# Kernel tuning notes

Measured on AMD Instinct MI355X. Metric: run time of the kernel, lower is better.

## Reference

```python
import jax, jax.numpy as jnp
import numpy as np

NINP, NC, NH = 34, 128, 512
B, S, T = 64, 2048, 400
EPS = 1e-10


def _lstm_cell(x, h, c, Wih, Whh, bih, bhh):
    # torch.nn.LSTMCell gate order: i, f, g, o
    g = x @ Wih.T + bih + h @ Whh.T + bhh
    i, f, gg, o = jnp.split(g, 4, axis=1)
    c2 = jax.nn.sigmoid(f) * c + jax.nn.sigmoid(i) * jnp.tanh(gg)
    h2 = jax.nn.sigmoid(o) * jnp.tanh(c2)
    return h2, c2


def _attend(keys, values, mask, query):
    # energy: [B, S]; mask: [B, S] float 0/1
    energy = jnp.einsum('bc,bsc->bs', query, keys) * mask
    energy = energy - (1.0 - mask) * 1e6
    e = jnp.exp(energy - energy.max(axis=1, keepdims=True)) * mask
    att = e / e.sum(axis=1, keepdims=True)
    ctx = jnp.einsum('bs,bsc->bc', att, values)
    return att, ctx


def setup_inputs() -> dict:
    key = jax.random.key(0)
    ks = jax.random.split(key, 32)
    def rn(k, shape, scale=0.05):
        return (jax.random.normal(k, shape) * scale).astype(jnp.float32)
    inp = {
        'keys': rn(ks[0], (B, S, NC), 1.0),
        'values': rn(ks[1], (B, S, NC), 1.0),
        'lens': jax.random.randint(ks[2], (B,), S // 2, S + 1),
        'inputs': jax.random.randint(ks[3], (B, T), 0, NINP),
        'emb': rn(ks[4], (NINP, NC)),
        'wq': rn(ks[5], (NC, NH)), 'bq': jnp.zeros((NC,), jnp.float32),
        'wc': rn(ks[6], (NC, NH + NC)), 'bc': jnp.zeros((NC,), jnp.float32),
        'b_out': jnp.zeros((NINP,), jnp.float32),
    }
    in_sizes = [2 * NC, NH, NH]
    for l in range(3):
        inp['w%d_ih' % l] = rn(ks[7 + 4 * l], (4 * NH, in_sizes[l]))
        inp['w%d_hh' % l] = rn(ks[8 + 4 * l], (4 * NH, NH))
        inp['b%d_ih' % l] = jnp.zeros((4 * NH,), jnp.float32)
        inp['b%d_hh' % l] = jnp.zeros((4 * NH,), jnp.float32)
        inp['h0_%d' % l] = jnp.zeros((NH,), jnp.float32)  # ALSTMCell h0 param (zero init)
        inp['c0_%d' % l] = jnp.zeros((NH,), jnp.float32)
    return inp


def reference(keys, values, lens, inputs, emb, wq, bq, wc, bc, b_out,
              w0_ih, w0_hh, b0_ih, b0_hh, h0_0, c0_0,
              w1_ih, w1_hh, b1_ih, b1_hh, h0_1, c0_1,
              w2_ih, w2_hh, b2_ih, b2_hh, h0_2, c0_2):
    mask = (jnp.arange(S)[None, :] < lens[:, None]).astype(keys.dtype)  # [B,S]
    h1 = jnp.broadcast_to(h0_0[None], (B, NH)); c1 = jnp.broadcast_to(c0_0[None], (B, NH))
    h2 = jnp.broadcast_to(h0_1[None], (B, NH)); c2 = jnp.broadcast_to(c0_1[None], (B, NH))
    h3 = jnp.broadcast_to(h0_2[None], (B, NH)); c3 = jnp.broadcast_to(c0_2[None], (B, NH))
    # initial attention from last layer's h0 (matches torch forward)
    query0 = h3 @ wq.T + bq
    _, ctx = _attend(keys, values, mask, query0)
    # precompute gumbel noise for all T steps: -log(eps - log(U + eps))
    U = jax.random.uniform(jax.random.key(1), (T, B, NINP), dtype=jnp.float32)
    gnoise = -jnp.log(EPS - jnp.log(U + EPS))

    def step(carry, xs):
        h1, c1, h2, c2, h3, c3, ctx = carry
        tok, gn = xs
        x = jnp.concatenate([emb[tok], ctx], axis=1)  # [B, 2*NC]
        h1, c1 = _lstm_cell(x, h1, c1, w0_ih, w0_hh, b0_ih, b0_hh)
        h2, c2 = _lstm_cell(h1, h2, c2, w1_ih, w1_hh, b1_ih, b1_hh)
        h3, c3 = _lstm_cell(h2, h3, c3, w2_ih, w2_hh, b2_ih, b2_hh)
        q = h3 @ wq.T + bq
        att, ctx = _attend(keys, values, mask, q)
        z = jax.nn.leaky_relu(jnp.concatenate([h3, ctx], axis=1) @ wc.T + bc, 0.01)
        logit = z @ emb.T + b_out  # tied output weight = embedding
        gen = jnp.argmax(logit + gn, axis=1)
        return (h1, c1, h2, c2, h3, c3, ctx), (logit, att, gen)

    _, (logits, attentions, generated) = jax.lax.scan(
        step, (h1, c1, h2, c2, h3, c3, ctx), (inputs.T, gnoise))
    return logits, attentions, generated
```

## Files before the change

kernel.cpp:

```cpp
#include <hip/hip_runtime.h>

#define NINP 34
#define NCC  128
#define NHH  512
#define BBB  64
#define SSS  2048
#define TTT  400
#define GEPS 1e-10f

#define GDIM 512
#define NTHR 256
#define NCHK 8
#define SCHK 256

#define JAX_PARTITIONABLE 1

#define OFF_H   0
#define OFF_C   196608
#define OFF_CTX 294912
#define OFF_ML  303104
#define OFF_P   303616

#define SY_ROOT 0
#define SY_GEN  16
#define SY_LEAFC(l) (256 + 8 * (l))
#define SY_LEAFG(l) (512 + 8 * (l))
#define SY_BF(b)    (1024 + 8 * (b))
#define SY_MF(b)    (1536 + 8 * (b))

struct Params {
  const float* keys; const float* values;
  const int* lens;  const int* toks;
  const float* emb; const float* wq; const float* bq;
  const float* wc;  const float* bc; const float* bout;
  const float* wih[3]; const float* whh[3];
  const float* bih[3]; const float* bhh[3];
  const float* h0[3];  const float* c0[3];
  float* out_logits; float* out_att; float* out_gen;
  float* wsf; unsigned* sync;
};

__device__ __forceinline__ float4 ld4(const float* p) { return *(const float4*)p; }
__device__ __forceinline__ float sigf(float x) { return 1.0f / (1.0f + expf(-x)); }

__device__ __forceinline__ unsigned aload(const unsigned* p) {
  return __hip_atomic_load(p, __ATOMIC_RELAXED, __HIP_MEMORY_SCOPE_AGENT);
}
__device__ __forceinline__ unsigned aadd(unsigned* p, unsigned v) {
  return __hip_atomic_fetch_add(p, v, __ATOMIC_RELAXED, __HIP_MEMORY_SCOPE_AGENT);
}
__device__ __forceinline__ void astore(unsigned* p, unsigned v) {
  __hip_atomic_store(p, v, __ATOMIC_RELAXED, __HIP_MEMORY_SCOPE_AGENT);
}
__device__ __forceinline__ float ldc(const float* p) {
  unsigned u = __hip_atomic_load((const unsigned*)p, __ATOMIC_RELAXED, __HIP_MEMORY_SCOPE_AGENT);
  return __uint_as_float(u);
}
__device__ __forceinline__ void stc(float* p, float v) {
  __hip_atomic_store((unsigned*)p, __float_as_uint(v), __ATOMIC_RELAXED, __HIP_MEMORY_SCOPE_AGENT);
}
__device__ __forceinline__ float4 ld4c(const float* p) {
  unsigned long long a = __hip_atomic_load((const unsigned long long*)p,
                                           __ATOMIC_RELAXED, __HIP_MEMORY_SCOPE_AGENT);
  unsigned long long b = __hip_atomic_load(((const unsigned long long*)p) + 1,
                                           __ATOMIC_RELAXED, __HIP_MEMORY_SCOPE_AGENT);
  float4 r;
  r.x = __uint_as_float((unsigned)a); r.y = __uint_as_float((unsigned)(a >> 32));
  r.z = __uint_as_float((unsigned)b); r.w = __uint_as_float((unsigned)(b >> 32));
  return r;
}
__device__ __forceinline__ void wait_vm0() {
  asm volatile("s_waitcnt vmcnt(0)" ::: "memory");
}
__device__ __forceinline__ void cbar() { asm volatile("" ::: "memory"); }

__device__ void gbar(unsigned* sync, unsigned& epoch, int bid) {
  wait_vm0();
  __syncthreads();
  if (threadIdx.x == 0) {
    epoch++;
    const int leaf = bid >> 4;
    const bool leader = (bid & 15) == 0;
    if (aadd(&sync[SY_LEAFC(leaf)], 1u) == 16u * epoch - 1u) {
      if (aadd(&sync[SY_ROOT], 1u) == 32u * epoch - 1u)
        astore(&sync[SY_GEN], epoch);
    }
    if (leader) {
      while (aload(&sync[SY_GEN]) < epoch) __builtin_amdgcn_s_sleep(1);
      astore(&sync[SY_LEAFG(leaf)], epoch);
    } else {
      while (aload(&sync[SY_LEAFG(leaf)]) < epoch) __builtin_amdgcn_s_sleep(1);
    }
  }
  __syncthreads();
  cbar();
}

__device__ __forceinline__ void waitflag(unsigned* p, unsigned target) {
  if (threadIdx.x == 0) {
    while (aload(p) < target) __builtin_amdgcn_s_sleep(2);
  }
  __syncthreads();
  cbar();
}
__device__ __forceinline__ void postflag(unsigned* p) {
  wait_vm0();
  __syncthreads();
  if (threadIdx.x == 0) aadd(p, 1u);
}

__device__ __forceinline__ void tfr(unsigned& x0, unsigned& x1, int r) {
  x0 += x1; x1 = (x1 << r) | (x1 >> (32 - r)); x1 ^= x0;
}
__device__ unsigned threefry_bits(unsigned idx) {
  const unsigned k0 = 0u, k1 = 1u;
  const unsigned k2 = 0x1BD11BDAu ^ k0 ^ k1;
#if JAX_PARTITIONABLE
  unsigned x0 = 0u, x1 = idx;
#else
  const unsigned half = (TTT * BBB * NINP) / 2;
  const bool lo = idx < half;
  unsigned x0 = lo ? idx : idx - half;
  unsigned x1 = lo ? idx + half : idx;
#endif
  x0 += k0; x1 += k1;
  tfr(x0,x1,13); tfr(x0,x1,15); tfr(x0,x1,26); tfr(x0,x1,6);
  x0 += k1; x1 += k2 + 1u;
  tfr(x0,x1,17); tfr(x0,x1,29); tfr(x0,x1,16); tfr(x0,x1,24);
  x0 += k2; x1 += k0 + 2u;
  tfr(x0,x1,13); tfr(x0,x1,15); tfr(x0,x1,26); tfr(x0,x1,6);
  x0 += k0; x1 += k1 + 3u;
  tfr(x0,x1,17); tfr(x0,x1,29); tfr(x0,x1,16); tfr(x0,x1,24);
  x0 += k1; x1 += k2 + 4u;
  tfr(x0,x1,13); tfr(x0,x1,15); tfr(x0,x1,26); tfr(x0,x1,6);
  x0 += k2; x1 += k0 + 5u;
#if JAX_PARTITIONABLE
  return x0 ^ x1;
#else
  return lo ? x0 : x1;
#endif
}
__device__ __forceinline__ float gumbel(unsigned idx) {
  unsigned bits = threefry_bits(idx);
  float u = __uint_as_float((bits >> 9) | 0x3f800000u) - 1.0f;
  u = fmaxf(u, 0.0f);
  return -logf(GEPS - logf(u + GEPS));
}

template<int L>
__device__ void lstm_layer(const Params& p, int t, const float* hin, float* hout,
                           float* sh, int up, int bh, int tid) {
  const float* hin_l = hin + L * BBB * NHH + (size_t)bh * 32 * NHH;
  float* houtl = hout + L * BBB * NHH;
  float* cl = p.wsf + OFF_C + L * BBB * NHH;
  const float* xlow = (L == 0) ? (const float*)0
                               : (hout + (L - 1) * BBB * NHH + (size_t)bh * 32 * NHH);

  const int insz = (L == 0) ? (2 * NCC) : NHH;
  const int nx = insz >> 7;
  const int nch = nx + 4;

  const int rhat = tid >> 5;
  const int bloc = tid & 31;
  const int g = rhat >> 1, jh = rhat & 1;
  const int j = 2 * up + jh;
  const int row = g * NHH + j;
  const float* wr  = p.wih[L] + (size_t)row * insz;
  const float* wr2 = p.whh[L] + (size_t)row * NHH;

  float* xb0 = sh;
  float* xb1 = sh + 4224;
  const int kk  = (tid & 31) << 2;
  const int rb0 = tid >> 5;

  float4 pf[4];
  auto issue = [&](int cc) {
#pragma unroll
    for (int it = 0; it < 4; ++it) {
      const int rb = rb0 + (it << 3);
      const int gb = bh * 32 + rb;
      const bool isx = cc < nx;
      const int off = (isx ? cc : cc - nx) << 7;
      if (L == 0) {
        if (isx) pf[it] = (cc == 0)
            ? ld4(p.emb + (size_t)p.toks[gb * TTT + t] * NCC + kk)
            : ld4c(p.wsf + OFF_CTX + gb * NCC + kk);
        else pf[it] = ld4c(hin_l + (size_t)rb * NHH + off + kk);
      } else {
        pf[it] = isx ? ld4c(xlow + (size_t)rb * NHH + off + kk)
                     : ld4c(hin_l + (size_t)rb * NHH + off + kk);
      }
    }
  };
  auto commit = [&](float* buf) {
#pragma unroll
    for (int it = 0; it < 4; ++it)
      *(float4*)&buf[(rb0 + (it << 3)) * 132 + kk] = pf[it];
  };

  float acc = p.bih[L][row] + p.bhh[L][row];
  float s0 = 0.f, s1 = 0.f, s2 = 0.f, s3 = 0.f;

  issue(0);
  commit(xb0);
  __syncthreads();
  for (int cc = 0; cc < nch; ++cc) {
    if (cc + 1 < nch) issue(cc + 1);
    const bool isx = cc < nx;
    const int off = (isx ? cc : cc - nx) << 7;
    const float* wp = (isx ? wr : wr2) + off;
    const float* xr = ((cc & 1) ? xb1 : xb0) + bloc * 132;
#pragma unroll 8
    for (int k = 0; k < 128; k += 4) {
      float4 w = ld4(wp + k);
      float4 x = ld4(xr + k);
      s0 = fmaf(w.x, x.x, s0); s1 = fmaf(w.y, x.y, s1);
      s2 = fmaf(w.z, x.z, s2); s3 = fmaf(w.w, x.w, s3);
    }
    if (cc + 1 < nch) commit((cc & 1) ? xb0 : xb1);
    __syncthreads();
  }
  acc += (s0 + s1) + (s2 + s3);

  float* gl = sh + 8448;
  gl[rhat * 32 + bloc] = acc;
  __syncthreads();
  if (tid < 64) {
    const int jh2 = tid >> 5, b2 = tid & 31;
    const int b = bh * 32 + b2;
    const int jj = 2 * up + jh2;
    const float iv = gl[(0 + jh2) * 32 + b2];
    const float fv = gl[(2 + jh2) * 32 + b2];
    const float gv = gl[(4 + jh2) * 32 + b2];
    const float ov = gl[(6 + jh2) * 32 + b2];
    const float cold = cl[(size_t)b * NHH + jj];
    const float cnew = sigf(fv) * cold + sigf(iv) * tanhf(gv);
    const float hnew = sigf(ov) * tanhf(cnew);
    cl[(size_t)b * NHH + jj] = cnew;
    stc(&houtl[(size_t)b * NHH + jj], hnew);
  }
}

__device__ void attend_phase(const Params& p, int a, int t, const float* h3,
                             float* sh, int bid, int tid, bool wout) {
  float* wsf = p.wsf;
  unsigned* sync = p.sync;
  const int b  = (bid & 7) * 8 + (bid >> 6);
  const int ch = (bid >> 3) & 7;
  const int sbase = ch * SCHK;

  float* us  = sh + 8704;
  float* qs  = sh + 9344;
  float* ps  = sh + 9472;
  float* red = sh + 9728;
  float* zs  = sh + 10784;
  float* lg  = sh + 10912;

  if (tid < 128) *(float4*)&us[tid * 4] = ld4c(h3 + (size_t)b * NHH + tid * 4);
  __syncthreads();
  if (tid < NCC) {
    const float* wr = p.wq + (size_t)tid * NHH;
    float s0 = 0.f, s1 = 0.f, s2 = 0.f, s3 = 0.f;
#pragma unroll 8
    for (int k = 0; k < NHH; k += 4) {
      float4 w = ld4(wr + k);
      s0 = fmaf(w.x, us[k],     s0); s1 = fmaf(w.y, us[k + 1], s1);
      s2 = fmaf(w.z, us[k + 2], s2); s3 = fmaf(w.w, us[k + 3], s3);
    }
    qs[tid] = p.bq[tid] + (s0 + s1) + (s2 + s3);
  }
  const int lenb = p.lens[b];
  __syncthreads();

  const int s = sbase + tid;
  const float* kr = p.keys + ((size_t)b * SSS + s) * NCC;
  float e0 = 0.f, e1 = 0.f, e2 = 0.f, e3 = 0.f;
#pragma unroll 8
  for (int c = 0; c < NCC; c += 4) {
    float4 kv = ld4(kr + c);
    e0 = fmaf(qs[c],     kv.x, e0); e1 = fmaf(qs[c + 1], kv.y, e1);
    e2 = fmaf(qs[c + 2], kv.z, e2); e3 = fmaf(qs[c + 3], kv.w, e3);
  }
  float e = (e0 + e1) + (e2 + e3);
  const bool msk = s < lenb;
  e = msk ? e : -1e6f;

  float mx = e;
#pragma unroll
  for (int off = 32; off; off >>= 1) mx = fmaxf(mx, __shfl_xor(mx, off));
  if ((tid & 63) == 0) red[tid >> 6] = mx;
  __syncthreads();
  const float mc = fmaxf(fmaxf(red[0], red[1]), fmaxf(red[2], red[3]));
  const float pv = msk ? expf(e - mc) : 0.f;
  ps[tid] = pv;
  float ls = pv;
#pragma unroll
  for (int off = 32; off; off >>= 1) ls += __shfl_xor(ls, off);
  if ((tid & 63) == 0) red[4 + (tid >> 6)] = ls;
  __syncthreads();
  const float lc = (red[4] + red[5]) + (red[6] + red[7]);

  const int c4 = (tid & 31) << 2;
  const int sg = tid >> 5;
  float r0 = 0.f, r1 = 0.f, r2 = 0.f, r3 = 0.f;
  const float* vb = p.values + ((size_t)b * SSS + sbase + sg * 32) * NCC + c4;
#pragma unroll 4
  for (int i2 = 0; i2 < 32; ++i2) {
    const float pw = ps[sg * 32 + i2];
    float4 vv = ld4(vb + (size_t)i2 * NCC);
    r0 = fmaf(pw, vv.x, r0); r1 = fmaf(pw, vv.y, r1);
    r2 = fmaf(pw, vv.z, r2); r3 = fmaf(pw, vv.w, r3);
  }
  __syncthreads();
  *(float4*)&red[sg * 132 + c4] = make_float4(r0, r1, r2, r3);
  __syncthreads();
  float* pout = wsf + OFF_P + ((size_t)b * NCHK + ch) * 132;
  if (tid < NCC) {
    float sum = 0.f;
#pragma unroll
    for (int sg2 = 0; sg2 < 8; ++sg2) sum += red[sg2 * 132 + tid];
    stc(&pout[4 + tid], sum);
  }
  if (tid == 0) { stc(&pout[0], mc); stc(&pout[1], lc); }
  postflag(&sync[SY_BF(b)]);

  float gm = 0.f, gL = 1.f;
  if (ch == 0) {
    waitflag(&sync[SY_BF(b)], (unsigned)(NCHK * (a + 1)));
    const float* pb = wsf + OFF_P + (size_t)b * NCHK * 132;
    if (tid < 8)       red[tid] = ldc(&pb[tid * 132]);
    else if (tid < 16) red[tid] = ldc(&pb[(tid - 8) * 132 + 1]);
    __syncthreads();
    float m = red[0];
#pragma unroll
    for (int i = 1; i < 8; ++i) m = fmaxf(m, red[i]);
    float L = 0.f;
#pragma unroll
    for (int i = 0; i < 8; ++i) L += red[8 + i] * expf(red[i] - m);
    gm = m; gL = L;
    if (tid < NCC) {
      float v = 0.f;
#pragma unroll
      for (int c2 = 0; c2 < NCHK; ++c2)
        v += ldc(&pb[c2 * 132 + 4 + tid]) * expf(red[c2] - m);
      v /= L;
      stc(&wsf[OFF_CTX + b * NCC + tid], v);
      us[NHH + tid] = v;
    }
    if (tid == 0) { stc(&wsf[OFF_ML + b * 8], m); stc(&wsf[OFF_ML + b * 8 + 1], L); }
    postflag(&sync[SY_MF(b)]);
  } else if (wout) {
    waitflag(&sync[SY_MF(b)], (unsigned)(a + 1));
    gm = ldc(&wsf[OFF_ML + b * 8]);
    gL = ldc(&wsf[OFF_ML + b * 8 + 1]);
  }

  if (wout) {
    float* ao = p.out_att + ((size_t)t * BBB + b) * SSS;
    ao[s] = (msk ? expf(e - gm) : 0.f) / gL;
    if (ch == 0) {
      if (tid < NCC) {
        const float* wr = p.wc + (size_t)tid * (NHH + NCC);
        float s0 = 0.f, s1 = 0.f, s2 = 0.f, s3 = 0.f;
#pragma unroll 8
        for (int k = 0; k < NHH + NCC; k += 4) {
          float4 w = ld4(wr + k);
          s0 = fmaf(w.x, us[k],     s0); s1 = fmaf(w.y, us[k + 1], s1);
          s2 = fmaf(w.z, us[k + 2], s2); s3 = fmaf(w.w, us[k + 3], s3);
        }
        float z = (s0 + s1) + (s2 + s3) + p.bc[tid];
        zs[tid] = (z >= 0.f) ? z : 0.01f * z;
      }
      __syncthreads();
      if (tid < NINP) {
        const float* er = p.emb + tid * NCC;
        float s0 = 0.f, s1 = 0.f, s2 = 0.f, s3 = 0.f;
#pragma unroll 8
        for (int k = 0; k < NCC; k += 4) {
          float4 w = ld4(er + k);
          s0 = fmaf(w.x, zs[k],     s0); s1 = fmaf(w.y, zs[k + 1], s1);
          s2 = fmaf(w.z, zs[k + 2], s2); s3 = fmaf(w.w, zs[k + 3], s3);
        }
        const float lgt = (s0 + s1) + (s2 + s3) + p.bout[tid];
        p.out_logits[((size_t)t * BBB + b) * NINP + tid] = lgt;
        lg[tid] = lgt + gumbel((unsigned)(t * (BBB * NINP) + b * NINP + tid));
      }
      __syncthreads();
      if (tid == 0) {
        float bv = lg[0]; int bix = 0;
        for (int i = 1; i < NINP; ++i) if (lg[i] > bv) { bv = lg[i]; bix = i; }
        p.out_gen[t * BBB + b] = (float)bix;
      }
    }
  }
}

extern "C" __global__ void __launch_bounds__(NTHR, 2)
decoder_kernel(Params p) {
  __shared__ float sh[11008];
  const int bid = blockIdx.x;
  const int tid = threadIdx.x;
  const int up = (bid & 7) * 32 + (bid >> 4);
  const int bh = (bid >> 3) & 1;
  unsigned epoch = 0;
  unsigned* sync = p.sync;
  float* wsf = p.wsf;

  if (tid < 192) {
    const int l = tid >> 6, u = tid & 63;
    const int jh = u >> 5, b2 = u & 31;
    const int b = bh * 32 + b2;
    const int j = 2 * up + jh;
    stc(&wsf[OFF_H + ((size_t)l * BBB + b) * NHH + j], p.h0[l][j]);
    wsf[OFF_C + ((size_t)l * BBB + b) * NHH + j] = p.c0[l][j];
  }
  gbar(sync, epoch, bid);

  attend_phase(p, 0, -1, wsf + OFF_H + 2 * BBB * NHH, sh, bid, tid, false);
  gbar(sync, epoch, bid);

  for (int t = 0; t < TTT; ++t) {
    const float* hin = wsf + OFF_H + ((t & 1) ? 3 * BBB * NHH : 0);
    float* hout      = wsf + OFF_H + ((t & 1) ? 0 : 3 * BBB * NHH);

    lstm_layer<0>(p, t, hin, hout, sh, up, bh, tid);
    gbar(sync, epoch, bid);
    lstm_layer<1>(p, t, hin, hout, sh, up, bh, tid);
    gbar(sync, epoch, bid);
    lstm_layer<2>(p, t, hin, hout, sh, up, bh, tid);
    gbar(sync, epoch, bid);
    attend_phase(p, t + 1, t, hout + 2 * BBB * NHH, sh, bid, tid, true);
    gbar(sync, epoch, bid);
  }
}

extern "C" void kernel_launch(void* const* d_in, const int* in_sizes, int n_in,
                              void* d_out, int out_size, void* d_ws, size_t ws_size,
                              hipStream_t stream) {
  Params p;
  p.keys   = (const float*)d_in[0];
  p.values = (const float*)d_in[1];
  p.lens   = (const int*)d_in[2];
  p.toks   = (const int*)d_in[3];
  p.emb    = (const float*)d_in[4];
  p.wq     = (const float*)d_in[5];
  p.bq     = (const float*)d_in[6];
  p.wc     = (const float*)d_in[7];
  p.bc     = (const float*)d_in[8];
  p.bout   = (const float*)d_in[9];
  for (int l = 0; l < 3; ++l) {
    p.wih[l] = (const float*)d_in[10 + 6 * l];
    p.whh[l] = (const float*)d_in[11 + 6 * l];
    p.bih[l] = (const float*)d_in[12 + 6 * l];
    p.bhh[l] = (const float*)d_in[13 + 6 * l];
    p.h0[l]  = (const float*)d_in[14 + 6 * l];
    p.c0[l]  = (const float*)d_in[15 + 6 * l];
  }
  float* out = (float*)d_out;
  p.out_logits = out;
  p.out_att    = out + (size_t)TTT * BBB * NINP;
  p.out_gen    = out + (size_t)TTT * BBB * NINP + (size_t)TTT * BBB * SSS;
  p.sync = (unsigned*)d_ws;
  p.wsf  = (float*)((char*)d_ws + 8192);

  hipMemsetAsync(d_ws, 0, 8192, stream);
  decoder_kernel<<<dim3(GDIM), dim3(NTHR), 0, stream>>>(p);
}
```

Measured before the change: 49.78 ms.

## Replace post-attention grid barrier with per-half context flags and triple-buffer LSTM staging

Removes the grid-wide barrier after each attention phase. Layer-0 LSTM blocks now wait on a per-batch-half counter that the attention merge blocks bump when they publish ctx, so layer 0 can start its hidden-state chunks before all attention work finishes. The LSTM input staging moves from double to triple buffering with two register prefetch sets, which deepens the prefetch and raises shared memory use. This risks less occupancy and ordering hazards, since attention-output blocks may still be running when the LSTM reuses shared memory and workspace.

```diff
diff --git a/kernel.cpp b/kernel.cpp
--- a/kernel.cpp
+++ b/kernel.cpp
@@ -25,6 +25,7 @@
 #define SY_GEN  16
 #define SY_LEAFC(l) (256 + 8 * (l))
 #define SY_LEAFG(l) (512 + 8 * (l))
+#define SY_CTXH(h)  (768 + 64 * (h))
 #define SY_BF(b)    (1024 + 8 * (b))
 #define SY_MF(b)    (1536 + 8 * (b))
 
@@ -107,6 +108,11 @@
   wait_vm0();
   __syncthreads();
   if (threadIdx.x == 0) aadd(p, 1u);
+}
+__device__ __forceinline__ void postflag2(unsigned* p0, unsigned* p1) {
+  wait_vm0();
+  __syncthreads();
+  if (threadIdx.x == 0) { aadd(p0, 1u); aadd(p1, 1u); }
 }
 
 __device__ __forceinline__ void tfr(unsigned& x0, unsigned& x1, int r) {
@@ -149,16 +155,16 @@
 
 template<int L>
 __device__ void lstm_layer(const Params& p, int t, const float* hin, float* hout,
-                           float* sh, int up, int bh, int tid) {
+                           float* sh, int up, int bh, int tid, unsigned* sync) {
   const float* hin_l = hin + L * BBB * NHH + (size_t)bh * 32 * NHH;
   float* houtl = hout + L * BBB * NHH;
   float* cl = p.wsf + OFF_C + L * BBB * NHH;
   const float* xlow = (L == 0) ? (const float*)0
                                : (hout + (L - 1) * BBB * NHH + (size_t)bh * 32 * NHH);
 
-  const int insz = (L == 0) ? (2 * NCC) : NHH;
-  const int nx = insz >> 7;
-  const int nch = nx + 4;
+  constexpr int insz = (L == 0) ? (2 * NCC) : NHH;
+  constexpr int nx = insz >> 7;
+  constexpr int nch = nx + 4;
 
   const int rhat = tid >> 5;
   const int bloc = tid & 31;
@@ -168,13 +174,14 @@
   const float* wr  = p.wih[L] + (size_t)row * insz;
   const float* wr2 = p.whh[L] + (size_t)row * NHH;
 
-  float* xb0 = sh;
-  float* xb1 = sh + 4224;
+  float* const xb0 = sh;
+  float* const xb1 = sh + 4224;
+  float* const xb2 = sh + 8448;
   const int kk  = (tid & 31) << 2;
   const int rb0 = tid >> 5;
 
-  float4 pf[4];
-  auto issue = [&](int cc) {
+  float4 pfA[4], pfB[4];
+  auto issue = [&](float4 (&pf)[4], int cc) {
 #pragma unroll
     for (int it = 0; it < 4; ++it) {
       const int rb = rb0 + (it << 3);
@@ -192,7 +199,7 @@
       }
     }
   };
-  auto commit = [&](float* buf) {
+  auto commit = [&](float4 (&pf)[4], float* buf) {
 #pragma unroll
     for (int it = 0; it < 4; ++it)
       *(float4*)&buf[(rb0 + (it << 3)) * 132 + kk] = pf[it];
@@ -201,15 +208,21 @@
   float acc = p.bih[L][row] + p.bhh[L][row];
   float s0 = 0.f, s1 = 0.f, s2 = 0.f, s3 = 0.f;
 
-  issue(0);
-  commit(xb0);
-  __syncthreads();
+  issue(pfA, 0);
+  if (L == 0) {
+    waitflag(&sync[SY_CTXH(bh)], 32u * (unsigned)(t + 1));
+  }
+  commit(pfA, xb0);
+  issue(pfB, 1);
+  __syncthreads();
+#pragma unroll
   for (int cc = 0; cc < nch; ++cc) {
-    if (cc + 1 < nch) issue(cc + 1);
+    if (cc + 2 < nch) issue((cc & 1) ? pfB : pfA, cc + 2);
     const bool isx = cc < nx;
     const int off = (isx ? cc : cc - nx) << 7;
     const float* wp = (isx ? wr : wr2) + off;
-    const float* xr = ((cc & 1) ? xb1 : xb0) + bloc * 132;
+    float* const bufc = (cc % 3 == 0) ? xb0 : (cc % 3 == 1) ? xb1 : xb2;
+    const float* xr = bufc + bloc * 132;
 #pragma unroll 8
     for (int k = 0; k < 128; k += 4) {
       float4 w = ld4(wp + k);
@@ -217,12 +230,15 @@
       s0 = fmaf(w.x, x.x, s0); s1 = fmaf(w.y, x.y, s1);
       s2 = fmaf(w.z, x.z, s2); s3 = fmaf(w.w, x.w, s3);
     }
-    if (cc + 1 < nch) commit((cc & 1) ? xb0 : xb1);
+    if (cc + 1 < nch) {
+      float* const bufn = ((cc + 1) % 3 == 0) ? xb0 : ((cc + 1) % 3 == 1) ? xb1 : xb2;
+      commit(((cc + 1) & 1) ? pfB : pfA, bufn);
+    }
     __syncthreads();
   }
   acc += (s0 + s1) + (s2 + s3);
 
-  float* gl = sh + 8448;
+  float* gl = sh + 12672;
   gl[rhat * 32 + bloc] = acc;
   __syncthreads();
   if (tid < 64) {
@@ -249,12 +265,12 @@
   const int ch = (bid >> 3) & 7;
   const int sbase = ch * SCHK;
 
-  float* us  = sh + 8704;
-  float* qs  = sh + 9344;
-  float* ps  = sh + 9472;
-  float* red = sh + 9728;
-  float* zs  = sh + 10784;
-  float* lg  = sh + 10912;
+  float* us  = sh + 12928;
+  float* qs  = sh + 13568;
+  float* ps  = sh + 13696;
+  float* red = sh + 13952;
+  float* zs  = sh + 15008;
+  float* lg  = sh + 15136;
 
   if (tid < 128) *(float4*)&us[tid * 4] = ld4c(h3 + (size_t)b * NHH + tid * 4);
   __syncthreads();
@@ -348,7 +364,7 @@
       us[NHH + tid] = v;
     }
     if (tid == 0) { stc(&wsf[OFF_ML + b * 8], m); stc(&wsf[OFF_ML + b * 8 + 1], L); }
-    postflag(&sync[SY_MF(b)]);
+    postflag2(&sync[SY_MF(b)], &sync[SY_CTXH(b >> 5)]);
   } else if (wout) {
     waitflag(&sync[SY_MF(b)], (unsigned)(a + 1));
     gm = ldc(&wsf[OFF_ML + b * 8]);
@@ -391,13 +407,14 @@
         for (int i = 1; i < NINP; ++i) if (lg[i] > bv) { bv = lg[i]; bix = i; }
         p.out_gen[t * BBB + b] = (float)bix;
       }
+      __syncthreads();
     }
   }
 }
 
 extern "C" __global__ void __launch_bounds__(NTHR, 2)
 decoder_kernel(Params p) {
-  __shared__ float sh[11008];
+  __shared__ float sh[15232];
   const int bid = blockIdx.x;
   const int tid = threadIdx.x;
   const int up = (bid & 7) * 32 + (bid >> 4);
@@ -417,20 +434,18 @@
   gbar(sync, epoch, bid);
 
   attend_phase(p, 0, -1, wsf + OFF_H + 2 * BBB * NHH, sh, bid, tid, false);
-  gbar(sync, epoch, bid);
 
   for (int t = 0; t < TTT; ++t) {
     const float* hin = wsf + OFF_H + ((t & 1) ? 3 * BBB * NHH : 0);
     float* hout      = wsf + OFF_H + ((t & 1) ? 0 : 3 * BBB * NHH);
 
-    lstm_layer<0>(p, t, hin, hout, sh, up, bh, tid);
+    lstm_layer<0>(p, t, hin, hout, sh, up, bh, tid, sync);
     gbar(sync, epoch, bid);
-    lstm_layer<1>(p, t, hin, hout, sh, up, bh, tid);
+    lstm_layer<1>(p, t, hin, hout, sh, up, bh, tid, sync);
     gbar(sync, epoch, bid);
-    lstm_layer<2>(p, t, hin, hout, sh, up, bh, tid);
+    lstm_layer<2>(p, t, hin, hout, sh, up, bh, tid, sync);
     gbar(sync, epoch, bid);
     attend_phase(p, t + 1, t, hout + 2 * BBB * NHH, sh, bid, tid, true);
-    gbar(sync, epoch, bid);
   }
 }
 
```

Measured after the change: 53.81 ms. +8.1%, slower.
